# Kernel tuning notes

Hardware: AMD Instinct MI355X
Metric: run time of the kernel (lower is better)

## Reference

```python
import jax, jax.numpy as jnp
import numpy as np
from jax import lax

NUM_CLASSES = 10
NUM_ITER = 3
DN = ('NCHW', 'OIHW', 'NCHW')


def squash(t, axis=-1):
    sq = (t ** 2).sum(axis=axis, keepdims=True)
    return (sq / (1.0 + sq)) * t / jnp.sqrt(sq)


def setup_inputs() -> dict:
    key = jax.random.key(0)
    ks = jax.random.split(key, 12)
    B = 512
    s = 0.05  # param scale for numerical stability
    return {
        'x': jax.random.normal(ks[0], (B, 1, 28, 28), jnp.float32),
        'conv1_w': jax.random.normal(ks[1], (256, 1, 9, 9), jnp.float32) * s,
        'conv1_b': jax.random.normal(ks[2], (256,), jnp.float32) * s,
        'prim_w': jax.random.normal(ks[3], (8, 32, 256, 9, 9), jnp.float32) * s,
        'prim_b': jax.random.normal(ks[4], (8, 32), jnp.float32) * s,
        'route_w': jax.random.normal(ks[5], (NUM_CLASSES, 32 * 6 * 6, 8, 16), jnp.float32),
        'dec_w1': jax.random.normal(ks[6], (512, 16 * NUM_CLASSES), jnp.float32) * s,
        'dec_b1': jax.random.normal(ks[7], (512,), jnp.float32) * s,
        'dec_w2': jax.random.normal(ks[8], (1024, 512), jnp.float32) * s,
        'dec_b2': jax.random.normal(ks[9], (1024,), jnp.float32) * s,
        'dec_w3': jax.random.normal(ks[10], (784, 1024), jnp.float32) * s,
        'dec_b3': jax.random.normal(ks[11], (784,), jnp.float32) * s,
    }


def reference(x, conv1_w, conv1_b, prim_w, prim_b, route_w,
              dec_w1, dec_b1, dec_w2, dec_b2, dec_w3, dec_b3):
    B = x.shape[0]
    # conv1 + relu: [B,256,20,20]
    h = lax.conv_general_dilated(x, conv1_w, (1, 1), 'VALID', dimension_numbers=DN)
    h = jax.nn.relu(h + conv1_b[None, :, None, None])
    # primary capsules: 8 parallel convs fused into one conv with 8*32 out channels
    kw = prim_w.reshape(8 * 32, 256, 9, 9)
    u = lax.conv_general_dilated(h, kw, (2, 2), 'VALID', dimension_numbers=DN)
    u = u + prim_b.reshape(-1)[None, :, None, None]          # [B,256,6,6]
    u = u.reshape(B, 8, 32 * 6 * 6).transpose(0, 2, 1)       # [B,1152,8]
    u = squash(u, axis=-1)
    # digit capsules: priors [C,B,R,16]
    priors = jnp.einsum('bri,crio->cbro', u, route_w)
    logits = jnp.zeros_like(priors)
    for i in range(NUM_ITER):
        probs = jax.nn.softmax(logits, axis=2)
        v = squash((probs * priors).sum(axis=2, keepdims=True))  # [C,B,1,16]
        if i != NUM_ITER - 1:
            logits = logits + (priors * v).sum(axis=-1, keepdims=True)
    caps = v.squeeze(2).transpose(1, 0, 2)                    # [B,C,16]
    classes = jnp.sqrt((caps ** 2).sum(axis=-1))              # [B,C]
    classes = jax.nn.softmax(classes, axis=1)
    y = jax.nn.one_hot(jnp.argmax(classes, axis=1), NUM_CLASSES, dtype=caps.dtype)
    d = (caps * y[:, :, None]).reshape(B, -1)                 # [B,160]
    d = jax.nn.relu(d @ dec_w1.T + dec_b1)
    d = jax.nn.relu(d @ dec_w2.T + dec_b2)
    recon = jax.nn.sigmoid(d @ dec_w3.T + dec_b3)             # [B,784]
    return classes, recon
```

## Files before the change

kernel.cpp:

```cpp
#include <hip/hip_runtime.h>
#include <math.h>


typedef _Float16 f16;
typedef _Float16 f16x8 __attribute__((ext_vector_type(8)));
typedef _Float16 f16x4 __attribute__((ext_vector_type(4)));
typedef float f32x4 __attribute__((ext_vector_type(4)));

__device__ __forceinline__ void gl_lds16(const void* g, void* l) {
  __builtin_amdgcn_global_load_lds(
      (const __attribute__((address_space(1))) void*)g,
      (__attribute__((address_space(3))) void*)l, 16, 0, 0);
}

__global__ __launch_bounds__(256, 2) void conv1_kernel(
    const float* __restrict__ x, const float* __restrict__ w,
    const float* __restrict__ bias, f16* __restrict__ ht)
{
  __shared__ float xs[784];
  const int b = blockIdx.x;
  const int t = threadIdx.x;
  for (int i = t; i < 784; i += 256) xs[i] = x[b * 784 + i];
  float wr[81];
#pragma unroll
  for (int k = 0; k < 81; ++k) wr[k] = w[t * 81 + k];
  const float bv = bias[t];
  __syncthreads();
  for (int oy = 0; oy < 20; ++oy) {
    float acc[20];
#pragma unroll
    for (int i = 0; i < 20; ++i) acc[i] = bv;
#pragma unroll
    for (int ky = 0; ky < 9; ++ky) {
      float xr[28];
#pragma unroll
      for (int q = 0; q < 7; ++q) {
        const float4 v = *(const float4*)&xs[(oy + ky) * 28 + q * 4];
        xr[q*4+0] = v.x; xr[q*4+1] = v.y; xr[q*4+2] = v.z; xr[q*4+3] = v.w;
      }
#pragma unroll
      for (int kx = 0; kx < 9; ++kx) {
        const float wv = wr[ky * 9 + kx];
#pragma unroll
        for (int ox = 0; ox < 20; ++ox) acc[ox] = fmaf(xr[ox + kx], wv, acc[ox]);
      }
    }
    f16* hp = &ht[(size_t)((b * 20 + oy) * 20) * 256 + t];
#pragma unroll
    for (int ox = 0; ox < 20; ++ox)
      hp[ox * 256] = (f16)fmaxf(acc[ox], 0.f);
  }
}

__global__ __launch_bounds__(256) void wtrans_kernel(
    const float* __restrict__ w, f16* __restrict__ wt)
{
  __shared__ float tile[64 * 83];
  const int oc = blockIdx.x;
  const int icq = blockIdx.y;
  const int t = threadIdx.x;
  const float* src = w + (size_t)oc * 20736 + (size_t)icq * 64 * 81;
  for (int idx = t; idx < 5184; idx += 256) {
    const int ici = idx / 81, kk = idx - ici * 81;
    tile[ici * 83 + kk] = src[idx];
  }
  __syncthreads();
  f16* dst = wt + (size_t)oc * 20736 + icq * 64;
  for (int idx = t; idx < 5184; idx += 256) {
    const int kk = idx >> 6, ici = idx & 63;
    dst[kk * 256 + ici] = (f16)tile[ici * 83 + kk];
  }
}

__global__ __launch_bounds__(256) void prim_mfma_kernel(
    const f16* __restrict__ ht, const f16* __restrict__ wt,
    float* __restrict__ part)
{
  __shared__ f16 sm[16384];
  const int t = threadIdx.x;
  const int wv = t >> 6, lane = t & 63;
  const int id = blockIdx.x;
  const int g = id >> 3;
  const int ks = g & 3;
  const int nb = (g >> 2) & 1;
  const int mb = (id & 7) + 8 * (g >> 3);
  const int m0 = mb * 128, n0 = nb * 128;

  const int chunk = (lane & 7) ^ ((lane >> 3) & 7);
  long aoff[4], boff[4];
#pragma unroll
  for (int i = 0; i < 4; ++i) {
    const int r = wv * 32 + i * 8 + (lane >> 3);
    const int m = m0 + r;
    const int b = m / 36, pos = m - b * 36;
    const int oy = pos / 6, ox = pos - oy * 6;
    aoff[i] = (long)(((b * 20 + 2 * oy) * 20 + 2 * ox) * 256) * 2 + chunk * 16;
    boff[i] = (long)(n0 + r) * 41472 + chunk * 16;
  }
  const char* htc = (const char*)ht;
  const char* wtc = (const char*)wt;

  const int lrow = lane & 15, quad = lane >> 4;
  const int wm = wv & 1, wn = wv >> 1;
  f32x4 acc[4][4] = {};

  const int s0 = ks * 81, s1 = s0 + 81;
  for (int s = s0; s < s1; ++s) {
    const int kykx = s >> 2, icb = s & 3;
    const int ky = kykx / 9, kx = kykx - ky * 9;
    const long astep = (long)((((ky * 20 + kx) * 256) + icb * 64) * 2);
    const long bstep = (long)(((kykx * 256) + icb * 64) * 2);
    __syncthreads();
    {
      char* dA = (char*)sm + wv * 4096;
      char* dB = (char*)sm + 16384 + wv * 4096;
#pragma unroll
      for (int i = 0; i < 4; ++i) {
        gl_lds16(htc + aoff[i] + astep, dA + i * 1024);
        gl_lds16(wtc + boff[i] + bstep, dB + i * 1024);
      }
    }
    __syncthreads();
    const f16* As = sm;
    const f16* Bs = sm + 8192;
#pragma unroll
    for (int h = 0; h < 2; ++h) {
      f16x8 af[4], bf[4];
      const int cbase = h * 4 + quad;
      const int cp = cbase ^ (lrow & 7);
#pragma unroll
      for (int mt = 0; mt < 4; ++mt)
        af[mt] = *(const f16x8*)&As[(wm * 64 + mt * 16 + lrow) * 64 + cp * 8];
#pragma unroll
      for (int nt = 0; nt < 4; ++nt)
        bf[nt] = *(const f16x8*)&Bs[(wn * 64 + nt * 16 + lrow) * 64 + cp * 8];
#pragma unroll
      for (int mt = 0; mt < 4; ++mt)
#pragma unroll
        for (int nt = 0; nt < 4; ++nt)
          acc[mt][nt] = __builtin_amdgcn_mfma_f32_16x16x32_f16(
              af[mt], bf[nt], acc[mt][nt], 0, 0, 0);
    }
  }

  float* pp = part + (size_t)ks * 4718592;
#pragma unroll
  for (int mt = 0; mt < 4; ++mt) {
    const int mbase = m0 + wm * 64 + mt * 16 + quad * 4;
#pragma unroll
    for (int nt = 0; nt < 4; ++nt) {
      const int n = n0 + wn * 64 + nt * 16 + lrow;
      const int np = (n & 31) * 8 + (n >> 5);
#pragma unroll
      for (int rg = 0; rg < 4; ++rg)
        pp[(size_t)(mbase + rg) * 256 + np] = acc[mt][nt][rg];
    }
  }
}

__global__ void squash_kernel(const float* __restrict__ part,
                              const float* __restrict__ bias,
                              float* __restrict__ u)
{
  const int tid = blockIdx.x * 256 + threadIdx.x;
  if (tid >= 512 * 36 * 32) return;
  const int cc = tid & 31;
  const int row = tid >> 5;
  const int b = row / 36;
  const int pos = row - b * 36;
  const float* p = part + (size_t)row * 256 + cc * 8;
  float v[8] = {};
#pragma unroll
  for (int ksl = 0; ksl < 4; ++ksl) {
    const float4 a0 = *(const float4*)(p + (size_t)ksl * 4718592);
    const float4 a1 = *(const float4*)(p + (size_t)ksl * 4718592 + 4);
    v[0] += a0.x; v[1] += a0.y; v[2] += a0.z; v[3] += a0.w;
    v[4] += a1.x; v[5] += a1.y; v[6] += a1.z; v[7] += a1.w;
  }
  float sq = 0.f;
#pragma unroll
  for (int i = 0; i < 8; ++i) {
    v[i] += bias[i * 32 + cc];
    sq = fmaf(v[i], v[i], sq);
  }
  const float scale = sq / ((1.f + sq) * sqrtf(sq));
  float* up = &u[(size_t)(b * 1152 + cc * 36 + pos) * 8];
#pragma unroll
  for (int i = 0; i < 8; ++i) up[i] = v[i] * scale;
}

__global__ __launch_bounds__(256, 4) void priors_kernel(
    const float* __restrict__ u, const float* __restrict__ rw,
    f16* __restrict__ P)
{
  const int t = threadIdx.x;
  const int rl = t >> 2, oq = t & 3;
  const int r = blockIdx.x * 64 + rl;
  const int b0 = blockIdx.y * 64;
  const int c = blockIdx.z;

  float4 wreg[8];
  const float* wbase = rw + (size_t)(c * 1152 + r) * 128 + oq * 4;
#pragma unroll
  for (int k = 0; k < 8; ++k)
    wreg[k] = *(const float4*)(wbase + k * 16);

  f16* pbase = P + (size_t)((c * 512 + b0) * 1152 + r) * 16 + oq * 4;
  const float* ubase = u + (size_t)(b0 * 1152 + r) * 8;

  for (int b = 0; b < 64; ++b) {
    const float4 ua = *(const float4*)(ubase + (size_t)b * 9216);
    const float4 ub = *(const float4*)(ubase + (size_t)b * 9216 + 4);
    const float uu[8] = {ua.x, ua.y, ua.z, ua.w, ub.x, ub.y, ub.z, ub.w};
    float ax = 0.f, ay = 0.f, az = 0.f, aw = 0.f;
#pragma unroll
    for (int k = 0; k < 8; ++k) {
      ax = fmaf(uu[k], wreg[k].x, ax);
      ay = fmaf(uu[k], wreg[k].y, ay);
      az = fmaf(uu[k], wreg[k].z, az);
      aw = fmaf(uu[k], wreg[k].w, aw);
    }
    f16x4 st;
    st[0] = (f16)ax; st[1] = (f16)ay; st[2] = (f16)az; st[3] = (f16)aw;
    *(f16x4*)(pbase + (size_t)b * 18432) = st;
  }
}

__device__ __forceinline__ float wave_sum(float v) {
#pragma unroll
  for (int off = 32; off > 0; off >>= 1) v += __shfl_xor(v, off);
  return v;
}
__device__ __forceinline__ float wave_max(float v) {
#pragma unroll
  for (int off = 32; off > 0; off >>= 1) v = fmaxf(v, __shfl_xor(v, off));
  return v;
}

__global__ __launch_bounds__(256, 2) void routing_kernel(
    const f16* __restrict__ Pg, float* __restrict__ caps)
{
  const int c = blockIdx.x >> 9;
  const int b = blockIdx.x & 511;
  const int t = threadIdx.x;
  const int wid = t >> 6;
  const int lane = t & 63;
  __shared__ float xred[4 * 17];

  float P[5][16];
  float lg[5];
  const int nk = (t < 128) ? 5 : 4;
#pragma unroll
  for (int k = 0; k < 5; ++k)
#pragma unroll
    for (int o = 0; o < 16; ++o) P[k][o] = 0.f;

  const f16* pbase = Pg + (size_t)((c * 512 + b) * 1152) * 16;
#pragma unroll
  for (int k = 0; k < 5; ++k) {
    if (k < nk) {
      const int r = t + (k << 8);
      const f16x8 p0 = *(const f16x8*)&pbase[(size_t)r * 16];
      const f16x8 p1 = *(const f16x8*)&pbase[(size_t)r * 16 + 8];
#pragma unroll
      for (int o = 0; o < 8; ++o) {
        P[k][o]     = (float)p0[o];
        P[k][o + 8] = (float)p1[o];
      }
    }
  }

  float v[16];
  {
    float sq = 0.f;
#pragma unroll
    for (int o = 0; o < 16; ++o) {
      float p = 0.f;
#pragma unroll
      for (int k = 0; k < 5; ++k) p += P[k][o];
      p = wave_sum(p);
      if (lane == 0) xred[wid * 17 + o] = p;
      v[o] = 0.f;
    }
    __syncthreads();
#pragma unroll
    for (int o = 0; o < 16; ++o) {
      const float s = (xred[o] + xred[17 + o] + xred[34 + o] + xred[51 + o]) *
                      (1.f / 1152.f);
      v[o] = s;
      sq = fmaf(s, s, sq);
    }
    const float scale = sq / ((1.f + sq) * sqrtf(sq));
#pragma unroll
    for (int o = 0; o < 16; ++o) v[o] *= scale;
    __syncthreads();
  }
#pragma unroll
  for (int k = 0; k < 5; ++k) {
    float a = 0.f;
#pragma unroll
    for (int o = 0; o < 16; ++o) a = fmaf(P[k][o], v[o], a);
    lg[k] = a;
  }

  for (int it = 1; it < 3; ++it) {
    float m = -1e30f;
#pragma unroll
    for (int k = 0; k < 5; ++k) if (k < nk) m = fmaxf(m, lg[k]);
    m = wave_max(m);
    if (lane == 0) xred[wid * 17 + 16] = m;
    __syncthreads();
    const float mx = fmaxf(fmaxf(xred[16], xred[17 + 16]),
                           fmaxf(xred[34 + 16], xred[51 + 16]));
    __syncthreads();
    float e[5];
#pragma unroll
    for (int k = 0; k < 5; ++k) e[k] = (k < nk) ? expf(lg[k] - mx) : 0.f;
    float pS = 0.f;
#pragma unroll
    for (int k = 0; k < 5; ++k) pS += e[k];
    pS = wave_sum(pS);
    if (lane == 0) xred[wid * 17 + 16] = pS;
#pragma unroll
    for (int o = 0; o < 16; ++o) {
      float p = 0.f;
#pragma unroll
      for (int k = 0; k < 5; ++k) p = fmaf(e[k], P[k][o], p);
      p = wave_sum(p);
      if (lane == 0) xred[wid * 17 + o] = p;
    }
    __syncthreads();
    const float S = xred[16] + xred[17 + 16] + xred[34 + 16] + xred[51 + 16];
    const float inv = 1.f / S;
    float sq = 0.f;
#pragma unroll
    for (int o = 0; o < 16; ++o) {
      const float s = (xred[o] + xred[17 + o] + xred[34 + o] + xred[51 + o]) * inv;
      v[o] = s;
      sq = fmaf(s, s, sq);
    }
    const float scale = sq / ((1.f + sq) * sqrtf(sq));
#pragma unroll
    for (int o = 0; o < 16; ++o) v[o] *= scale;
    __syncthreads();
    if (it < 2) {
#pragma unroll
      for (int k = 0; k < 5; ++k) {
        float a = 0.f;
#pragma unroll
        for (int o = 0; o < 16; ++o) a = fmaf(P[k][o], v[o], a);
        lg[k] += a;
      }
    }
  }
  if (t == 0) {
    float* cp = &caps[(b * 10 + c) * 16];
#pragma unroll
    for (int o = 0; o < 16; ++o) cp[o] = v[o];
  }
}

__global__ void classes_kernel(const float* __restrict__ caps,
                               float* __restrict__ out_classes,
                               float* __restrict__ d0)
{
  const int b = blockIdx.x * 256 + threadIdx.x;
  if (b >= 512) return;
  float nrm[10];
#pragma unroll
  for (int cc = 0; cc < 10; ++cc) {
    float sq = 0.f;
#pragma unroll
    for (int o = 0; o < 16; ++o) {
      const float vv = caps[(b * 10 + cc) * 16 + o];
      sq = fmaf(vv, vv, sq);
    }
    nrm[cc] = sqrtf(sq);
  }
  float mx = nrm[0]; int cs = 0;
#pragma unroll
  for (int cc = 1; cc < 10; ++cc)
    if (nrm[cc] > mx) { mx = nrm[cc]; cs = cc; }
  float e[10], ssum = 0.f;
#pragma unroll
  for (int cc = 0; cc < 10; ++cc) { e[cc] = expf(nrm[cc] - mx); ssum += e[cc]; }
  const float inv = 1.f / ssum;
#pragma unroll
  for (int cc = 0; cc < 10; ++cc) out_classes[b * 10 + cc] = e[cc] * inv;
#pragma unroll
  for (int cc = 0; cc < 10; ++cc)
#pragma unroll
    for (int o = 0; o < 16; ++o)
      d0[b * 160 + cc * 16 + o] = (cc == cs) ? caps[(b * 10 + cc) * 16 + o] : 0.f;
}

__global__ __launch_bounds__(256, 2) void fc_kernel(
    const float* __restrict__ A, const float* __restrict__ W,
    const float* __restrict__ bias, float* __restrict__ C,
    int N, int K, int act)
{
  __shared__ float As[64][17];
  __shared__ float Ws[64][17];
  const int t = threadIdx.x;
  const int tm = t >> 4, tn = t & 15;
  const int m0 = blockIdx.y << 6, n0 = blockIdx.x << 6;
  const int lr = t >> 2, lq = (t & 3) << 2;
  float acc[4][4] = {};
  for (int k0 = 0; k0 < K; k0 += 16) {
    const float4 av = *(const float4*)&A[(m0 + lr) * K + k0 + lq];
    float4 wv = make_float4(0.f, 0.f, 0.f, 0.f);
    const int wn = n0 + lr;
    if (wn < N) wv = *(const float4*)&W[wn * K + k0 + lq];
    __syncthreads();
    As[lr][lq+0] = av.x; As[lr][lq+1] = av.y; As[lr][lq+2] = av.z; As[lr][lq+3] = av.w;
    Ws[lr][lq+0] = wv.x; Ws[lr][lq+1] = wv.y; Ws[lr][lq+2] = wv.z; Ws[lr][lq+3] = wv.w;
    __syncthreads();
#pragma unroll
    for (int kk = 0; kk < 16; ++kk) {
      float a[4], w[4];
#pragma unroll
      for (int i = 0; i < 4; ++i) a[i] = As[tm * 4 + i][kk];
#pragma unroll
      for (int j = 0; j < 4; ++j) w[j] = Ws[tn * 4 + j][kk];
#pragma unroll
      for (int i = 0; i < 4; ++i)
#pragma unroll
        for (int j = 0; j < 4; ++j) acc[i][j] = fmaf(a[i], w[j], acc[i][j]);
    }
  }
#pragma unroll
  for (int i = 0; i < 4; ++i) {
    const int m = m0 + tm * 4 + i;
#pragma unroll
    for (int j = 0; j < 4; ++j) {
      const int n = n0 + tn * 4 + j;
      if (n < N) {
        float vv = acc[i][j] + bias[n];
        vv = act ? (1.f / (1.f + expf(-vv))) : fmaxf(vv, 0.f);
        C[m * N + n] = vv;
      }
    }
  }
}

extern "C" void kernel_launch(void* const* d_in, const int* in_sizes, int n_in,
                              void* d_out, int out_size, void* d_ws, size_t ws_size,
                              hipStream_t stream)
{
  const float* x       = (const float*)d_in[0];
  const float* conv1_w = (const float*)d_in[1];
  const float* conv1_b = (const float*)d_in[2];
  const float* prim_w  = (const float*)d_in[3];
  const float* prim_b  = (const float*)d_in[4];
  const float* route_w = (const float*)d_in[5];
  const float* dec_w1  = (const float*)d_in[6];
  const float* dec_b1  = (const float*)d_in[7];
  const float* dec_w2  = (const float*)d_in[8];
  const float* dec_b2  = (const float*)d_in[9];
  const float* dec_w3  = (const float*)d_in[10];
  const float* dec_b3  = (const float*)d_in[11];
  float* out = (float*)d_out;

  char* ws = (char*)d_ws;
  f16*   ht   = (f16*)(ws);
  f16*   wtp  = (f16*)(ws + 104857600);
  float* part = (float*)(ws + 115474432);
  float* u    = (float*)(ws + 190971904);
  f16*   P    = (f16*)(ws);
  float* caps = (float*)(ws + 209846272);
  float* d0   = (float*)(ws + 210173952);
  float* d1   = (float*)(ws + 210501632);
  float* d2   = (float*)(ws + 211550208);

  hipLaunchKernelGGL(conv1_kernel, dim3(512), dim3(256), 0, stream,
                     x, conv1_w, conv1_b, ht);
  hipLaunchKernelGGL(wtrans_kernel, dim3(256, 4), dim3(256), 0, stream,
                     prim_w, wtp);
  hipLaunchKernelGGL(prim_mfma_kernel, dim3(1152), dim3(256), 0, stream,
                     ht, wtp, part);
  hipLaunchKernelGGL(squash_kernel, dim3(2304), dim3(256), 0, stream,
                     part, prim_b, u);
  hipLaunchKernelGGL(priors_kernel, dim3(18, 8, 10), dim3(256), 0, stream,
                     u, route_w, P);
  hipLaunchKernelGGL(routing_kernel, dim3(5120), dim3(256), 0, stream,
                     P, caps);
  hipLaunchKernelGGL(classes_kernel, dim3(2), dim3(256), 0, stream,
                     caps, out, d0);
  hipLaunchKernelGGL(fc_kernel, dim3(8, 8), dim3(256), 0, stream,
                     d0, dec_w1, dec_b1, d1, 512, 160, 0);
  hipLaunchKernelGGL(fc_kernel, dim3(16, 8), dim3(256), 0, stream,
                     d1, dec_w2, dec_b2, d2, 1024, 512, 0);
  hipLaunchKernelGGL(fc_kernel, dim3(13, 8), dim3(256), 0, stream,
                     d2, dec_w3, dec_b3, out + 5120, 784, 1024, 1);
}
```

Before: 841.5 us.

## Double-buffer prim MFMA LDS stages and split conv1 across row blocks

The primary-capsule MFMA GEMM now uses two LDS buffers with half-width K stages (32 channels). Global-to-LDS loads for the next stage are issued before the MFMAs on the current stage, to hide load latency behind compute. The swizzle is adjusted for the 32-wide rows. conv1 is also split into 4 row-blocks per image, raising the block count to improve occupancy. In exchange, conv1 reloads the weights per block and the GEMM runs more iterations with smaller stages.

```diff
diff --git a/kernel.cpp b/kernel.cpp
--- a/kernel.cpp
+++ b/kernel.cpp
@@ -17,16 +17,17 @@
     const float* __restrict__ x, const float* __restrict__ w,
     const float* __restrict__ bias, f16* __restrict__ ht)
 {
-  __shared__ float xs[784];
+  __shared__ float xs[364];
   const int b = blockIdx.x;
+  const int y0 = blockIdx.y * 5;
   const int t = threadIdx.x;
-  for (int i = t; i < 784; i += 256) xs[i] = x[b * 784 + i];
+  for (int i = t; i < 364; i += 256) xs[i] = x[b * 784 + y0 * 28 + i];
   float wr[81];
 #pragma unroll
   for (int k = 0; k < 81; ++k) wr[k] = w[t * 81 + k];
   const float bv = bias[t];
   __syncthreads();
-  for (int oy = 0; oy < 20; ++oy) {
+  for (int oy = y0; oy < y0 + 5; ++oy) {
     float acc[20];
 #pragma unroll
     for (int i = 0; i < 20; ++i) acc[i] = bv;
@@ -35,7 +36,7 @@
       float xr[28];
 #pragma unroll
       for (int q = 0; q < 7; ++q) {
-        const float4 v = *(const float4*)&xs[(oy + ky) * 28 + q * 4];
+        const float4 v = *(const float4*)&xs[(oy - y0 + ky) * 28 + q * 4];
         xr[q*4+0] = v.x; xr[q*4+1] = v.y; xr[q*4+2] = v.z; xr[q*4+3] = v.w;
       }
 #pragma unroll
@@ -86,11 +87,11 @@
   const int mb = (id & 7) + 8 * (g >> 3);
   const int m0 = mb * 128, n0 = nb * 128;
 
-  const int chunk = (lane & 7) ^ ((lane >> 3) & 7);
-  long aoff[4], boff[4];
-#pragma unroll
-  for (int i = 0; i < 4; ++i) {
-    const int r = wv * 32 + i * 8 + (lane >> 3);
+  const int chunk = (lane & 3) ^ ((lane >> 3) & 3);
+  long aoff[2], boff[2];
+#pragma unroll
+  for (int i = 0; i < 2; ++i) {
+    const int r = wv * 32 + i * 16 + (lane >> 2);
     const int m = m0 + r;
     const int b = m / 36, pos = m - b * 36;
     const int oy = pos / 6, ox = pos - oy * 6;
@@ -101,47 +102,52 @@
   const char* wtc = (const char*)wt;
 
   const int lrow = lane & 15, quad = lane >> 4;
+  const int qx = quad ^ ((lrow >> 1) & 3);
   const int wm = wv & 1, wn = wv >> 1;
   f32x4 acc[4][4] = {};
 
-  const int s0 = ks * 81, s1 = s0 + 81;
-  for (int s = s0; s < s1; ++s) {
-    const int kykx = s >> 2, icb = s & 3;
-    const int ky = kykx / 9, kx = kykx - ky * 9;
-    const long astep = (long)((((ky * 20 + kx) * 256) + icb * 64) * 2);
-    const long bstep = (long)(((kykx * 256) + icb * 64) * 2);
-    __syncthreads();
-    {
-      char* dA = (char*)sm + wv * 4096;
-      char* dB = (char*)sm + 16384 + wv * 4096;
-#pragma unroll
-      for (int i = 0; i < 4; ++i) {
-        gl_lds16(htc + aoff[i] + astep, dA + i * 1024);
-        gl_lds16(wtc + boff[i] + bstep, dB + i * 1024);
-      }
-    }
-    __syncthreads();
-    const f16* As = sm;
-    const f16* Bs = sm + 8192;
-#pragma unroll
-    for (int h = 0; h < 2; ++h) {
-      f16x8 af[4], bf[4];
-      const int cbase = h * 4 + quad;
-      const int cp = cbase ^ (lrow & 7);
-#pragma unroll
-      for (int mt = 0; mt < 4; ++mt)
-        af[mt] = *(const f16x8*)&As[(wm * 64 + mt * 16 + lrow) * 64 + cp * 8];
-#pragma unroll
-      for (int nt = 0; nt < 4; ++nt)
-        bf[nt] = *(const f16x8*)&Bs[(wn * 64 + nt * 16 + lrow) * 64 + cp * 8];
-#pragma unroll
-      for (int mt = 0; mt < 4; ++mt)
-#pragma unroll
-        for (int nt = 0; nt < 4; ++nt)
-          acc[mt][nt] = __builtin_amdgcn_mfma_f32_16x16x32_f16(
-              af[mt], bf[nt], acc[mt][nt], 0, 0, 0);
-    }
-  }
+  const int s0 = ks * 162, s1 = s0 + 162;
+
+#define STAGE(S, BUFB)                                                        \
+  {                                                                           \
+    const int kykx = (S) >> 3, icb = (S) & 7;                                 \
+    const int ky = kykx / 9, kx = kykx - ky * 9;                              \
+    const long astep = (long)((((ky * 20 + kx) * 256) + icb * 32) * 2);       \
+    const long bstep = (long)(((kykx * 256) + icb * 32) * 2);                 \
+    char* dA = (char*)sm + (BUFB) + wv * 2048;                                \
+    char* dB = (char*)sm + (BUFB) + 8192 + wv * 2048;                         \
+    gl_lds16(htc + aoff[0] + astep, dA);                                      \
+    gl_lds16(htc + aoff[1] + astep, dA + 1024);                               \
+    gl_lds16(wtc + boff[0] + bstep, dB);                                      \
+    gl_lds16(wtc + boff[1] + bstep, dB + 1024);                               \
+  }
+
+#define CONSUME(BUFI)                                                         \
+  {                                                                           \
+    const f16* As = sm + (BUFI);                                              \
+    const f16* Bs = sm + (BUFI) + 4096;                                       \
+    f16x8 af[4], bf[4];                                                       \
+    _Pragma("unroll") for (int mt = 0; mt < 4; ++mt)                          \
+        af[mt] = *(const f16x8*)&As[(wm * 64 + mt * 16 + lrow) * 32 + qx * 8];\
+    _Pragma("unroll") for (int nt = 0; nt < 4; ++nt)                          \
+        bf[nt] = *(const f16x8*)&Bs[(wn * 64 + nt * 16 + lrow) * 32 + qx * 8];\
+    _Pragma("unroll") for (int mt = 0; mt < 4; ++mt)                          \
+        _Pragma("unroll") for (int nt = 0; nt < 4; ++nt)                      \
+            acc[mt][nt] = __builtin_amdgcn_mfma_f32_16x16x32_f16(             \
+                af[mt], bf[nt], acc[mt][nt], 0, 0, 0);                        \
+  }
+
+  STAGE(s0, 0);
+  for (int s = s0; s < s1; s += 2) {
+    __syncthreads();
+    STAGE(s + 1, 16384);
+    CONSUME(0);
+    __syncthreads();
+    if (s + 2 < s1) STAGE(s + 2, 0);
+    CONSUME(8192);
+  }
+#undef STAGE
+#undef CONSUME
 
   float* pp = part + (size_t)ks * 4718592;
 #pragma unroll
@@ -472,7 +478,7 @@
   float* d1   = (float*)(ws + 210501632);
   float* d2   = (float*)(ws + 211550208);
 
-  hipLaunchKernelGGL(conv1_kernel, dim3(512), dim3(256), 0, stream,
+  hipLaunchKernelGGL(conv1_kernel, dim3(512, 4), dim3(256), 0, stream,
                      x, conv1_w, conv1_b, ht);
   hipLaunchKernelGGL(wtrans_kernel, dim3(256, 4), dim3(256), 0, stream,
                      prim_w, wtp);
```

New measurement: 799.7 us. -5.0%, faster.
